# Kernel tuning notes

Hardware: AMD Instinct MI355X
Metric: run time of the kernel (lower is better)

## Reference

```python
import jax, jax.numpy as jnp
import numpy as np

N_NODES = 50000
N_EDGES = 800000
D = 64  # node_dim == edge_dim
NEG_SLOPE = 0.2
EPS = 1e-5


def _lin_params(key, d_in, d_out):
    k1, k2 = jax.random.split(key)
    bound = 1.0 / np.sqrt(d_in)
    W = jax.random.uniform(k1, (d_out, d_in), minval=-bound, maxval=bound, dtype=jnp.float32)
    b = jax.random.uniform(k2, (d_out,), minval=-bound, maxval=bound, dtype=jnp.float32)
    return W, b


def setup_inputs() -> dict:
    key = jax.random.key(0)
    ks = jax.random.split(key, 12)
    V = jax.random.normal(ks[0], (N_NODES, D), dtype=jnp.float32)
    E = jax.random.normal(ks[1], (N_EDGES, D), dtype=jnp.float32)
    src = jax.random.randint(ks[2], (N_EDGES,), 0, N_NODES, dtype=jnp.int32)
    dst = jax.random.randint(ks[3], (N_EDGES,), 0, N_NODES, dtype=jnp.int32)
    pA_w, pA_b = _lin_params(ks[4], D, D)   # NodePooling.A
    pB_w, pB_b = _lin_params(ks[5], D, D)   # NodePooling.B
    mW1, mb1 = _lin_params(ks[6], D, D)     # edge MLP layer 1
    mW2, mb2 = _lin_params(ks[7], D, D)     # edge MLP layer 2
    BW, Bb = _lin_params(ks[8], D, D)       # GenMessage.B (scale)
    CW, Cb = _lin_params(ks[9], D, D)       # GenMessage.C (shift)
    return {"V": V, "E": E, "src": src, "dst": dst,
            "pA_w": pA_w, "pA_b": pA_b, "pB_w": pB_w, "pB_b": pB_b,
            "mW1": mW1, "mb1": mb1, "mW2": mW2, "mb2": mb2,
            "BW": BW, "Bb": Bb, "CW": CW, "Cb": Cb}


def _lrelu(x):
    return jnp.where(x >= 0, x, NEG_SLOPE * x)


def reference(V, E, src, dst, pA_w, pA_b, pB_w, pB_b, mW1, mb1, mW2, mb2, BW, Bb, CW, Cb):
    n = V.shape[0]
    # V = act(V); NodePooling: B(lrelu(A(V)))
    Va = _lrelu(V)
    Vp = _lrelu(Va @ pA_w.T + pA_b) @ pB_w.T + pB_b  # [N, D]
    # edge MLP on edge features (2 Linear+ReLU layers)
    x = jax.nn.relu(E @ mW1.T + mb1)
    x = jax.nn.relu(x @ mW2.T + mb2)                  # [E, D]
    scale = jax.nn.sigmoid(x @ BW.T + Bb)
    shift = x @ CW.T + Cb
    # gathered src features, gated affine message
    M1 = scale * Vp[src] + shift                      # [E, D]
    M2 = M1 * M1
    # segment-mean onto dst (DGL fn.mean); zero for isolated nodes
    deg = jax.ops.segment_sum(jnp.ones((dst.shape[0],), jnp.float32), dst, num_segments=n)
    denom = jnp.maximum(deg, 1.0)[:, None]
    V1 = jax.ops.segment_sum(M1, dst, num_segments=n) / denom
    V2 = jax.ops.segment_sum(M2, dst, num_segments=n) / denom
    return jnp.sqrt(jax.nn.relu(V2 - V1) + EPS)
```

## Files before the change

### kernel.cpp

```cpp
#include <hip/hip_runtime.h>

#define NN 50000
#define NE 800000
#define DDIM 64
#define PADX 68
#define PADS 68
#define NB_SCAN ((NN + 255) / 256)
#define NEG_SLOPE 0.2f
#define EPS_V 1e-5f

typedef short bf16x8 __attribute__((ext_vector_type(8)));
typedef float f32x4 __attribute__((ext_vector_type(4)));

__device__ __forceinline__ float lrelu_f(float x) { return x >= 0.0f ? x : NEG_SLOPE * x; }

__device__ __forceinline__ unsigned short bf16_rn(float x) {
    union { float f; unsigned int u; } c; c.f = x;
    unsigned int r = c.u + 0x7FFF + ((c.u >> 16) & 1);
    return (unsigned short)(r >> 16);
}
__device__ __forceinline__ float bf16_tof(unsigned short h) {
    union { float f; unsigned int u; } c; c.u = ((unsigned int)h) << 16;
    return c.f;
}

__device__ __forceinline__ unsigned cvtpk_bf16(float a, float b) {
    unsigned r;
    asm("v_cvt_pk_bf16_f32 %0, %1, %2" : "=v"(r) : "v"(a), "v"(b));
    return r;
}

__device__ __forceinline__ void split8(const float* __restrict__ v, bf16x8& h, bf16x8& l)
{
    union { bf16x8 v8; unsigned u[4]; } H, L;
    #pragma unroll
    for (int k = 0; k < 4; ++k) {
        float a = v[2*k], b = v[2*k+1];
        unsigned p = cvtpk_bf16(a, b);
        union { float f; unsigned u; } h0, h1;
        h0.u = p << 16;
        h1.u = p & 0xFFFF0000u;
        unsigned q = cvtpk_bf16(a - h0.f, b - h1.f);
        H.u[k] = p;
        L.u[k] = q;
    }
    h = H.v8; l = L.v8;
}

__device__ __forceinline__ void mma_tile(float acc[16], const float* __restrict__ XT,
                                         const float* __restrict__ Wc, int e0, int f0)
{
    #pragma unroll 4
    for (int kk = 0; kk < DDIM; kk += 4) {
        float4 A0 = *(const float4*)&XT[(kk+0)*PADX + e0];
        float4 A1 = *(const float4*)&XT[(kk+1)*PADX + e0];
        float4 A2 = *(const float4*)&XT[(kk+2)*PADX + e0];
        float4 A3 = *(const float4*)&XT[(kk+3)*PADX + e0];
        float4 B0 = *(const float4*)&Wc[(f0+0)*PADX + kk];
        float4 B1 = *(const float4*)&Wc[(f0+1)*PADX + kk];
        float4 B2 = *(const float4*)&Wc[(f0+2)*PADX + kk];
        float4 B3 = *(const float4*)&Wc[(f0+3)*PADX + kk];
        const float a[4][4] = {{A0.x,A0.y,A0.z,A0.w},{A1.x,A1.y,A1.z,A1.w},
                               {A2.x,A2.y,A2.z,A2.w},{A3.x,A3.y,A3.z,A3.w}};
        const float b[4][4] = {{B0.x,B0.y,B0.z,B0.w},{B1.x,B1.y,B1.z,B1.w},
                               {B2.x,B2.y,B2.z,B2.w},{B3.x,B3.y,B3.z,B3.w}};
        #pragma unroll
        for (int j = 0; j < 4; ++j)
            #pragma unroll
            for (int i = 0; i < 4; ++i)
                #pragma unroll
                for (int q = 0; q < 4; ++q)
                    acc[i*4+j] = fmaf(a[q][i], b[j][q], acc[i*4+j]);
    }
}

__device__ __forceinline__ void load_w_f32(float* __restrict__ Wc, const float* __restrict__ Wg, int tid)
{
    #pragma unroll
    for (int c = 0; c < 4; ++c) {
        int idx = (c << 10) + (tid << 2);
        int f = idx >> 6, k = idx & 63;
        *(float4*)&Wc[f*PADX + k] = *(const float4*)&Wg[idx];
    }
}

__global__ __launch_bounds__(256, 3)
void node_pool_kernel(const float* __restrict__ V,
                      const float* __restrict__ Aw, const float* __restrict__ Ab,
                      const float* __restrict__ Bw, const float* __restrict__ Bbv,
                      float* __restrict__ Vp,
                      const int* __restrict__ dst, int* __restrict__ degi)
{
    __shared__ float Wc[DDIM*PADX];
    __shared__ float XT[DDIM*PADX];
    const int tid = threadIdx.x;
    const int nb = blockIdx.x * 64;
    const int e0 = (tid & 15) << 2;
    const int f0 = (tid >> 4) << 2;

    #pragma unroll
    for (int c = 0; c < 4; ++c) {
        int idx = (c << 10) + (tid << 2);
        int e = idx >> 6, d = idx & 63;
        int row = nb + e; if (row > NN-1) row = NN-1;
        float4 v = *(const float4*)&V[(size_t)row*DDIM + d];
        XT[(d+0)*PADX + e] = lrelu_f(v.x);
        XT[(d+1)*PADX + e] = lrelu_f(v.y);
        XT[(d+2)*PADX + e] = lrelu_f(v.z);
        XT[(d+3)*PADX + e] = lrelu_f(v.w);
    }
    load_w_f32(Wc, Aw, tid);
    __syncthreads();

    float acc[16];
    #pragma unroll
    for (int i = 0; i < 16; ++i) acc[i] = 0.f;
    mma_tile(acc, XT, Wc, e0, f0);
    __syncthreads();

    {
        float4 bv = *(const float4*)&Ab[f0];
        const float ba[4] = {bv.x, bv.y, bv.z, bv.w};
        #pragma unroll
        for (int j = 0; j < 4; ++j) {
            float4 v;
            v.x = lrelu_f(acc[0*4+j] + ba[j]);
            v.y = lrelu_f(acc[1*4+j] + ba[j]);
            v.z = lrelu_f(acc[2*4+j] + ba[j]);
            v.w = lrelu_f(acc[3*4+j] + ba[j]);
            *(float4*)&XT[(f0+j)*PADX + e0] = v;
        }
    }
    load_w_f32(Wc, Bw, tid);
    __syncthreads();

    float acc2[16];
    #pragma unroll
    for (int i = 0; i < 16; ++i) acc2[i] = 0.f;
    mma_tile(acc2, XT, Wc, e0, f0);

    float4 bv = *(const float4*)&Bbv[f0];
    #pragma unroll
    for (int i = 0; i < 4; ++i) {
        int row = nb + e0 + i;
        if (row < NN) {
            float4 o;
            o.x = acc2[i*4+0] + bv.x;
            o.y = acc2[i*4+1] + bv.y;
            o.z = acc2[i*4+2] + bv.z;
            o.w = acc2[i*4+3] + bv.w;
            *(float4*)&Vp[(size_t)row*DDIM + f0] = o;
        }
    }

    const int stride = gridDim.x * 256;
    for (int e = blockIdx.x * 256 + tid; e < NE; e += stride)
        atomicAdd(&degi[dst[e]], 1);
}

__global__ __launch_bounds__(256)
void prep_w_kernel(const float* __restrict__ W1, const float* __restrict__ W2,
                   const float* __restrict__ WB, const float* __restrict__ WC,
                   short* __restrict__ WF)
{
    int gid = blockIdx.x * 256 + threadIdx.x;
    int L = gid >> 12, r = gid & 4095;
    int t = r >> 10, ks = (r >> 9) & 1, lane = (r >> 3) & 63, j = r & 7;
    const float* Ws = (L == 0) ? W1 : (L == 1) ? W2 : (L == 2) ? WB : WC;
    int n = lane & 15, kg = lane >> 4;
    int f = t*16 + n, k = ks*32 + kg*8 + j;
    float v = Ws[f*64 + k];
    unsigned short h = bf16_rn(v);
    unsigned short l = bf16_rn(v - bf16_tof(h));
    int base = L*8192 + ((t*2 + ks)*2)*512 + lane*8 + j;
    WF[base]       = (short)h;
    WF[base + 512] = (short)l;
}

__global__ __launch_bounds__(256)
void scan1_kernel(const int* __restrict__ degi, int* __restrict__ linc, int* __restrict__ bsum)
{
    __shared__ int ws[4];
    const int tid = threadIdx.x;
    const int lane = tid & 63, wv = tid >> 6;
    int i = blockIdx.x * 256 + tid;
    int v = (i < NN) ? degi[i] : 0;
    int sc = v;
    #pragma unroll
    for (int off = 1; off < 64; off <<= 1) {
        int t = __shfl_up(sc, off, 64);
        if (lane >= off) sc += t;
    }
    if (lane == 63) ws[wv] = sc;
    __syncthreads();
    int wb = 0;
    #pragma unroll
    for (int w = 0; w < 4; ++w) if (w < wv) wb += ws[w];
    int incl = sc + wb;
    if (i < NN) linc[i] = incl;
    if (tid == 255) bsum[blockIdx.x] = incl;
}

__global__ __launch_bounds__(256)
void scan23_kernel(const int* __restrict__ degi, const int* __restrict__ linc,
                   const int* __restrict__ bsum, int* __restrict__ curs)
{
    __shared__ int ws[4];
    __shared__ int base_s;
    const int tid = threadIdx.x;
    const int lane = tid & 63, wv = tid >> 6;
    int v = (tid < NB_SCAN) ? bsum[tid] : 0;
    int sc = v;
    #pragma unroll
    for (int off = 1; off < 64; off <<= 1) {
        int t = __shfl_up(sc, off, 64);
        if (lane >= off) sc += t;
    }
    if (lane == 63) ws[wv] = sc;
    __syncthreads();
    int wb = 0;
    #pragma unroll
    for (int w = 0; w < 4; ++w) if (w < wv) wb += ws[w];
    if (tid == blockIdx.x) base_s = sc + wb - v;
    __syncthreads();
    int i = blockIdx.x * 256 + tid;
    if (i < NN) curs[i] = base_s + linc[i] - degi[i];
}

__global__ __launch_bounds__(256)
void scatter_kernel(const int* __restrict__ dst, int* __restrict__ cursor, int* __restrict__ pinv)
{
    int e = blockIdx.x * 256 + threadIdx.x;
    if (e < NE) {
        pinv[e] = atomicAdd(&cursor[dst[e]], 1);
    }
}

__device__ __forceinline__ void gemm64_dual(const short* __restrict__ WL, int lane,
                                            const bf16x8 ah0[2], const bf16x8 al0[2],
                                            const bf16x8 ah1[2], const bf16x8 al1[2],
                                            f32x4 acc0[4], f32x4 acc1[4])
{
    #pragma unroll
    for (int ks = 0; ks < 2; ++ks) {
        bf16x8 bh[4], bl[4];
        #pragma unroll
        for (int t = 0; t < 4; ++t) {
            bh[t] = *(const bf16x8*)&WL[(((t*2 + ks)*2 + 0)*64 + lane)*8];
            bl[t] = *(const bf16x8*)&WL[(((t*2 + ks)*2 + 1)*64 + lane)*8];
        }
        #pragma unroll
        for (int t = 0; t < 4; ++t) {
            acc0[t] = __builtin_amdgcn_mfma_f32_16x16x32_bf16(al0[ks], bh[t], acc0[t], 0, 0, 0);
            acc1[t] = __builtin_amdgcn_mfma_f32_16x16x32_bf16(al1[ks], bh[t], acc1[t], 0, 0, 0);
            acc0[t] = __builtin_amdgcn_mfma_f32_16x16x32_bf16(ah0[ks], bl[t], acc0[t], 0, 0, 0);
            acc1[t] = __builtin_amdgcn_mfma_f32_16x16x32_bf16(ah1[ks], bl[t], acc1[t], 0, 0, 0);
            acc0[t] = __builtin_amdgcn_mfma_f32_16x16x32_bf16(ah0[ks], bh[t], acc0[t], 0, 0, 0);
            acc1[t] = __builtin_amdgcn_mfma_f32_16x16x32_bf16(ah1[ks], bh[t], acc1[t], 0, 0, 0);
        }
    }
}

__device__ __forceinline__ void gemm64(const short* __restrict__ WL, int lane,
                                       const bf16x8 ah[2], const bf16x8 al[2], f32x4 acc[4])
{
    #pragma unroll
    for (int ks = 0; ks < 2; ++ks) {
        bf16x8 bh[4], bl[4];
        #pragma unroll
        for (int t = 0; t < 4; ++t) {
            bh[t] = *(const bf16x8*)&WL[(((t*2 + ks)*2 + 0)*64 + lane)*8];
            bl[t] = *(const bf16x8*)&WL[(((t*2 + ks)*2 + 1)*64 + lane)*8];
        }
        #pragma unroll
        for (int t = 0; t < 4; ++t) {
            acc[t] = __builtin_amdgcn_mfma_f32_16x16x32_bf16(al[ks], bh[t], acc[t], 0, 0, 0);
            acc[t] = __builtin_amdgcn_mfma_f32_16x16x32_bf16(ah[ks], bl[t], acc[t], 0, 0, 0);
            acc[t] = __builtin_amdgcn_mfma_f32_16x16x32_bf16(ah[ks], bh[t], acc[t], 0, 0, 0);
        }
    }
}

__device__ __forceinline__ void transpose_frags(float* __restrict__ sw, const f32x4 y[4],
                                                int lane, bf16x8 ah[2], bf16x8 al[2])
{
    const int n = lane & 15, mg = lane >> 4;
    #pragma unroll
    for (int t = 0; t < 4; ++t)
        #pragma unroll
        for (int r = 0; r < 4; ++r)
            sw[(mg*4 + r)*PADS + t*16 + n] = y[t][r];
    __builtin_amdgcn_wave_barrier();
    const int m = lane & 15, kg = lane >> 4;
    float x[16];
    *(float4*)&x[0]  = *(const float4*)&sw[m*PADS + kg*8];
    *(float4*)&x[4]  = *(const float4*)&sw[m*PADS + kg*8 + 4];
    *(float4*)&x[8]  = *(const float4*)&sw[m*PADS + 32 + kg*8];
    *(float4*)&x[12] = *(const float4*)&sw[m*PADS + 32 + kg*8 + 4];
    split8(&x[0], ah[0], al[0]);
    split8(&x[8], ah[1], al[1]);
    __builtin_amdgcn_wave_barrier();
}

__global__ __launch_bounds__(256, 4)
void e1_mlp_kernel(const float* __restrict__ Eg,
                   const int* __restrict__ src, const int* __restrict__ pinv,
                   const short* __restrict__ WF,
                   const float* __restrict__ b1, const float* __restrict__ b2,
                   const float* __restrict__ bB, const float* __restrict__ bC,
                   const float* __restrict__ Vp,
                   float* __restrict__ M1s)
{
    __shared__ float scratch[4 * 16 * PADS];
    __shared__ int aux[4 * 64];

    const int tid = threadIdx.x;
    const int lane = tid & 63, wv = tid >> 6;
    float* sw = scratch + wv * 16 * PADS;
    int* auxw = aux + wv * 64;

    const int e0 = blockIdx.x * 128 + wv * 32;
    const int m = lane & 15, kg = lane >> 4;
    const int n = lane & 15, mg = lane >> 4;

    if (lane < 32) {
        auxw[lane]      = pinv[e0 + lane];
        auxw[32 + lane] = src[e0 + lane];
    }
    bf16x8 ah0[2], al0[2], ah1[2], al1[2];
    {
        const float* er0 = Eg + (size_t)(e0 + m)*DDIM + kg*8;
        const float* er1 = Eg + (size_t)(e0 + 16 + m)*DDIM + kg*8;
        float x[16];
        *(float4*)&x[0]  = *(const float4*)&er0[0];
        *(float4*)&x[4]  = *(const float4*)&er0[4];
        *(float4*)&x[8]  = *(const float4*)&er0[32];
        *(float4*)&x[12] = *(const float4*)&er0[36];
        split8(&x[0], ah0[0], al0[0]);
        split8(&x[8], ah0[1], al0[1]);
        *(float4*)&x[0]  = *(const float4*)&er1[0];
        *(float4*)&x[4]  = *(const float4*)&er1[4];
        *(float4*)&x[8]  = *(const float4*)&er1[32];
        *(float4*)&x[12] = *(const float4*)&er1[36];
        split8(&x[0], ah1[0], al1[0]);
        split8(&x[8], ah1[1], al1[1]);
    }

    f32x4 acc0[4], acc1[4];
    #pragma unroll
    for (int t = 0; t < 4; ++t) { acc0[t] = (f32x4){0.f,0.f,0.f,0.f}; acc1[t] = (f32x4){0.f,0.f,0.f,0.f}; }
    gemm64_dual(WF, lane, ah0, al0, ah1, al1, acc0, acc1);
    #pragma unroll
    for (int t = 0; t < 4; ++t) {
        float b = b1[t*16 + n];
        #pragma unroll
        for (int r = 0; r < 4; ++r) {
            acc0[t][r] = fmaxf(acc0[t][r] + b, 0.0f);
            acc1[t][r] = fmaxf(acc1[t][r] + b, 0.0f);
        }
    }
    transpose_frags(sw, acc0, lane, ah0, al0);
    transpose_frags(sw, acc1, lane, ah1, al1);

    #pragma unroll
    for (int t = 0; t < 4; ++t) { acc0[t] = (f32x4){0.f,0.f,0.f,0.f}; acc1[t] = (f32x4){0.f,0.f,0.f,0.f}; }
    gemm64_dual(WF + 8192, lane, ah0, al0, ah1, al1, acc0, acc1);
    #pragma unroll
    for (int t = 0; t < 4; ++t) {
        float b = b2[t*16 + n];
        #pragma unroll
        for (int r = 0; r < 4; ++r) {
            acc0[t][r] = fmaxf(acc0[t][r] + b, 0.0f);
            acc1[t][r] = fmaxf(acc1[t][r] + b, 0.0f);
        }
    }
    transpose_frags(sw, acc0, lane, ah0, al0);
    transpose_frags(sw, acc1, lane, ah1, al1);

    #pragma unroll
    for (int tile = 0; tile < 2; ++tile) {
        const int to = tile * 16;
        const bf16x8* ah = tile ? ah1 : ah0;
        const bf16x8* al = tile ? al1 : al0;

        f32x4 accS[4], accH[4];
        #pragma unroll
        for (int t = 0; t < 4; ++t) { accS[t] = (f32x4){0.f,0.f,0.f,0.f}; accH[t] = (f32x4){0.f,0.f,0.f,0.f}; }
        gemm64(WF + 2*8192, lane, ah, al, accS);
        gemm64(WF + 3*8192, lane, ah, al, accH);

        {
            int sn[4];
            #pragma unroll
            for (int r = 0; r < 4; ++r) sn[r] = auxw[32 + to + mg*4 + r];
            #pragma unroll
            for (int t = 0; t < 4; ++t) {
                const int ff = t*16 + n;
                const float bBv = bB[ff];
                const float bCv = bC[ff];
                #pragma unroll
                for (int r = 0; r < 4; ++r) {
                    float vp = Vp[(size_t)sn[r]*DDIM + ff];
                    float sg = 1.0f / (1.0f + __expf(-(accS[t][r] + bBv)));
                    sw[(mg*4 + r)*PADS + ff] = fmaf(sg, vp, accH[t][r] + bCv);
                }
            }
        }
        __builtin_amdgcn_wave_barrier();

        #pragma unroll 4
        for (int r = 0; r < 16; ++r) {
            int p = auxw[to + r];
            M1s[(size_t)p*DDIM + lane] = sw[r*PADS + lane];
        }
        __builtin_amdgcn_wave_barrier();
    }
}

__global__ __launch_bounds__(256)
void e2_reduce_kernel(const float* __restrict__ M1s,
                      const int* __restrict__ cend, const int* __restrict__ degi,
                      float* __restrict__ out)
{
    const int nw = blockIdx.x * 4 + (threadIdx.x >> 6);
    if (nw >= NN) return;
    const int lane = threadIdx.x & 63;
    const int deg = degi[nw];
    const int start = cend[nw] - deg;
    const float* base = M1s + (size_t)start*DDIM + lane;
    float s1 = 0.f, s2 = 0.f;
    int i = 0;
    for (; i + 4 <= deg; i += 4) {
        float a = base[(size_t)(i+0)*DDIM];
        float b = base[(size_t)(i+1)*DDIM];
        float c = base[(size_t)(i+2)*DDIM];
        float d = base[(size_t)(i+3)*DDIM];
        s1 += a + b + c + d;
        s2 = fmaf(a, a, s2); s2 = fmaf(b, b, s2);
        s2 = fmaf(c, c, s2); s2 = fmaf(d, d, s2);
    }
    for (; i < deg; ++i) {
        float a = base[(size_t)i*DDIM];
        s1 += a;
        s2 = fmaf(a, a, s2);
    }
    float dn = deg > 1 ? (float)deg : 1.0f;
    float v = (s2 - s1) / dn;
    out[(size_t)nw*DDIM + lane] = sqrtf(fmaxf(v, 0.0f) + EPS_V);
}

extern "C" void kernel_launch(void* const* d_in, const int* in_sizes, int n_in,
                              void* d_out, int out_size, void* d_ws, size_t ws_size,
                              hipStream_t stream) {
    const float* V   = (const float*)d_in[0];
    const float* Eg  = (const float*)d_in[1];
    const int*   src = (const int*)d_in[2];
    const int*   dst = (const int*)d_in[3];
    const float* pAw = (const float*)d_in[4];
    const float* pAb = (const float*)d_in[5];
    const float* pBw = (const float*)d_in[6];
    const float* pBb = (const float*)d_in[7];
    const float* mW1 = (const float*)d_in[8];
    const float* mb1 = (const float*)d_in[9];
    const float* mW2 = (const float*)d_in[10];
    const float* mb2 = (const float*)d_in[11];
    const float* BW  = (const float*)d_in[12];
    const float* Bb  = (const float*)d_in[13];
    const float* CW  = (const float*)d_in[14];
    const float* Cb  = (const float*)d_in[15];
    float* out = (float*)d_out;

    float* ws    = (float*)d_ws;
    float* Vp    = ws;
    int*   degi  = (int*)(ws + (size_t)NN*DDIM);
    int*   curs  = degi + NN;
    int*   linc  = curs + NN;
    int*   bsum  = linc + NN;
    int*   pinv  = bsum + NB_SCAN;
    short* WF    = (short*)(pinv + NE);
    float* M1s   = (float*)(WF + 4*8192);

    hipMemsetAsync(degi, 0, (size_t)NN * sizeof(int), stream);

    prep_w_kernel<<<64, 256, 0, stream>>>(mW1, mW2, BW, CW, WF);
    node_pool_kernel<<<(NN + 63)/64, 256, 0, stream>>>(V, pAw, pAb, pBw, pBb, Vp, dst, degi);
    scan1_kernel<<<NB_SCAN, 256, 0, stream>>>(degi, linc, bsum);
    scan23_kernel<<<NB_SCAN, 256, 0, stream>>>(degi, linc, bsum, curs);
    scatter_kernel<<<(NE + 255)/256, 256, 0, stream>>>(dst, curs, pinv);
    e1_mlp_kernel<<<NE/128, 256, 0, stream>>>(Eg, src, pinv, WF,
                                              mb1, mb2, Bb, Cb, Vp, M1s);
    e2_reduce_kernel<<<(NN + 3)/4, 256, 0, stream>>>(M1s, curs, degi, out);
}
```

Before: 598.4 us.

## Stage per-layer MLP weights in LDS and batch scale/shift GEMMs over both tiles

Each block now copies each 16 KB bf16 weight layer (hi/lo fragments) from global memory into a shared-memory buffer, guarded by block barriers, before running the MFMA GEMMs. Previously every wave read those weights straight from global or L2. The scale and shift GEMMs for both 16-row tiles are now computed up front with the dual-tile routine, so the separate single-tile GEMM is gone. This adds four block-wide syncs plus load phases per block, raises register pressure from holding four accumulator sets, and lowers the occupancy hint from 4 to 3 blocks.

```diff
diff --git a/kernel.cpp b/kernel.cpp
--- a/kernel.cpp
+++ b/kernel.cpp
@@ -236,18 +236,18 @@
     }
 }
 
-__device__ __forceinline__ void gemm64_dual(const short* __restrict__ WL, int lane,
-                                            const bf16x8 ah0[2], const bf16x8 al0[2],
-                                            const bf16x8 ah1[2], const bf16x8 al1[2],
-                                            f32x4 acc0[4], f32x4 acc1[4])
+__device__ __forceinline__ void gemm64_dual_lds(const short* bw, int lane,
+                                                const bf16x8 ah0[2], const bf16x8 al0[2],
+                                                const bf16x8 ah1[2], const bf16x8 al1[2],
+                                                f32x4 acc0[4], f32x4 acc1[4])
 {
     #pragma unroll
     for (int ks = 0; ks < 2; ++ks) {
         bf16x8 bh[4], bl[4];
         #pragma unroll
         for (int t = 0; t < 4; ++t) {
-            bh[t] = *(const bf16x8*)&WL[(((t*2 + ks)*2 + 0)*64 + lane)*8];
-            bl[t] = *(const bf16x8*)&WL[(((t*2 + ks)*2 + 1)*64 + lane)*8];
+            bh[t] = *(const bf16x8*)&bw[(((t*2 + ks)*2 + 0)*64 + lane)*8];
+            bl[t] = *(const bf16x8*)&bw[(((t*2 + ks)*2 + 1)*64 + lane)*8];
         }
         #pragma unroll
         for (int t = 0; t < 4; ++t) {
@@ -257,26 +257,6 @@
             acc1[t] = __builtin_amdgcn_mfma_f32_16x16x32_bf16(ah1[ks], bl[t], acc1[t], 0, 0, 0);
             acc0[t] = __builtin_amdgcn_mfma_f32_16x16x32_bf16(ah0[ks], bh[t], acc0[t], 0, 0, 0);
             acc1[t] = __builtin_amdgcn_mfma_f32_16x16x32_bf16(ah1[ks], bh[t], acc1[t], 0, 0, 0);
-        }
-    }
-}
-
-__device__ __forceinline__ void gemm64(const short* __restrict__ WL, int lane,
-                                       const bf16x8 ah[2], const bf16x8 al[2], f32x4 acc[4])
-{
-    #pragma unroll
-    for (int ks = 0; ks < 2; ++ks) {
-        bf16x8 bh[4], bl[4];
-        #pragma unroll
-        for (int t = 0; t < 4; ++t) {
-            bh[t] = *(const bf16x8*)&WL[(((t*2 + ks)*2 + 0)*64 + lane)*8];
-            bl[t] = *(const bf16x8*)&WL[(((t*2 + ks)*2 + 1)*64 + lane)*8];
-        }
-        #pragma unroll
-        for (int t = 0; t < 4; ++t) {
-            acc[t] = __builtin_amdgcn_mfma_f32_16x16x32_bf16(al[ks], bh[t], acc[t], 0, 0, 0);
-            acc[t] = __builtin_amdgcn_mfma_f32_16x16x32_bf16(ah[ks], bl[t], acc[t], 0, 0, 0);
-            acc[t] = __builtin_amdgcn_mfma_f32_16x16x32_bf16(ah[ks], bh[t], acc[t], 0, 0, 0);
         }
     }
 }
@@ -302,7 +282,7 @@
     __builtin_amdgcn_wave_barrier();
 }
 
-__global__ __launch_bounds__(256, 4)
+__global__ __launch_bounds__(256, 3)
 void e1_mlp_kernel(const float* __restrict__ Eg,
                    const int* __restrict__ src, const int* __restrict__ pinv,
                    const short* __restrict__ WF,
@@ -311,6 +291,7 @@
                    const float* __restrict__ Vp,
                    float* __restrict__ M1s)
 {
+    __shared__ short bw[8192];
     __shared__ float scratch[4 * 16 * PADS];
     __shared__ int aux[4 * 64];
 
@@ -322,6 +303,16 @@
     const int e0 = blockIdx.x * 128 + wv * 32;
     const int m = lane & 15, kg = lane >> 4;
     const int n = lane & 15, mg = lane >> 4;
+
+    auto load_layer = [&](const short* Wg) {
+        __syncthreads();
+        const uint4* s = (const uint4*)Wg;
+        uint4* d = (uint4*)bw;
+        #pragma unroll
+        for (int c = 0; c < 4; ++c)
+            d[c*256 + tid] = s[c*256 + tid];
+        __syncthreads();
+    };
 
     if (lane < 32) {
         auxw[lane]      = pinv[e0 + lane];
@@ -346,10 +337,11 @@
         split8(&x[8], ah1[1], al1[1]);
     }
 
+    load_layer(WF);
     f32x4 acc0[4], acc1[4];
     #pragma unroll
     for (int t = 0; t < 4; ++t) { acc0[t] = (f32x4){0.f,0.f,0.f,0.f}; acc1[t] = (f32x4){0.f,0.f,0.f,0.f}; }
-    gemm64_dual(WF, lane, ah0, al0, ah1, al1, acc0, acc1);
+    gemm64_dual_lds(bw, lane, ah0, al0, ah1, al1, acc0, acc1);
     #pragma unroll
     for (int t = 0; t < 4; ++t) {
         float b = b1[t*16 + n];
@@ -362,9 +354,10 @@
     transpose_frags(sw, acc0, lane, ah0, al0);
     transpose_frags(sw, acc1, lane, ah1, al1);
 
+    load_layer(WF + 8192);
     #pragma unroll
     for (int t = 0; t < 4; ++t) { acc0[t] = (f32x4){0.f,0.f,0.f,0.f}; acc1[t] = (f32x4){0.f,0.f,0.f,0.f}; }
-    gemm64_dual(WF + 8192, lane, ah0, al0, ah1, al1, acc0, acc1);
+    gemm64_dual_lds(bw, lane, ah0, al0, ah1, al1, acc0, acc1);
     #pragma unroll
     for (int t = 0; t < 4; ++t) {
         float b = b2[t*16 + n];
@@ -377,17 +370,23 @@
     transpose_frags(sw, acc0, lane, ah0, al0);
     transpose_frags(sw, acc1, lane, ah1, al1);
 
+    f32x4 accS0[4], accS1[4];
+    load_layer(WF + 2*8192);
+    #pragma unroll
+    for (int t = 0; t < 4; ++t) { accS0[t] = (f32x4){0.f,0.f,0.f,0.f}; accS1[t] = (f32x4){0.f,0.f,0.f,0.f}; }
+    gemm64_dual_lds(bw, lane, ah0, al0, ah1, al1, accS0, accS1);
+
+    f32x4 accH0[4], accH1[4];
+    load_layer(WF + 3*8192);
+    #pragma unroll
+    for (int t = 0; t < 4; ++t) { accH0[t] = (f32x4){0.f,0.f,0.f,0.f}; accH1[t] = (f32x4){0.f,0.f,0.f,0.f}; }
+    gemm64_dual_lds(bw, lane, ah0, al0, ah1, al1, accH0, accH1);
+
     #pragma unroll
     for (int tile = 0; tile < 2; ++tile) {
         const int to = tile * 16;
-        const bf16x8* ah = tile ? ah1 : ah0;
-        const bf16x8* al = tile ? al1 : al0;
-
-        f32x4 accS[4], accH[4];
-        #pragma unroll
-        for (int t = 0; t < 4; ++t) { accS[t] = (f32x4){0.f,0.f,0.f,0.f}; accH[t] = (f32x4){0.f,0.f,0.f,0.f}; }
-        gemm64(WF + 2*8192, lane, ah, al, accS);
-        gemm64(WF + 3*8192, lane, ah, al, accH);
+        f32x4* accS = tile ? accS1 : accS0;
+        f32x4* accH = tile ? accH1 : accH0;
 
         {
             int sn[4];
```

Result: faster. 535.1 us (-10.6%).
